# Optimization experiments

Measured on AMD Instinct MI355X. Metric: run time of the kernel, lower is better.

The kernel has to match this reference:

```python
import jax, jax.numpy as jnp
import numpy as np

K = 8            # NEAREST_K
IN = 68          # input_size = 64 + 4
EO = 32          # edge_output_size
FEAT = IN * 2 + EO * 4  # 264
EMB = 32         # linear_embedding
NCLS = 2
N = 768
EPS = 1e-5


def lrelu(x):
    return jnp.where(x >= 0, x, 0.01 * x)


def setup_inputs() -> dict:
    key = jax.random.key(0)
    ks = jax.random.split(key, 16)

    def w(k, fan_in, fan_out):
        return jax.random.normal(k, (fan_in, fan_out), jnp.float32) / np.float32(np.sqrt(fan_in))

    return {
        "feat0": jax.random.normal(ks[0], (N, IN), jnp.float32),
        "feat1": jax.random.normal(ks[1], (N, IN), jnp.float32),
        # edge_conv1: Linear(IN*K, EO) -> LeakyReLU -> Linear(EO, EO) -> LeakyReLU
        "ec1_w1": w(ks[2], IN * K, EO), "ec1_b1": jnp.zeros((EO,), jnp.float32),
        "ec1_w2": w(ks[3], EO, EO),     "ec1_b2": jnp.zeros((EO,), jnp.float32),
        # edge_conv2: Linear(EO*K, EO) -> LeakyReLU -> Linear(EO, EO) -> LeakyReLU
        "ec2_w1": w(ks[4], EO * K, EO), "ec2_b1": jnp.zeros((EO,), jnp.float32),
        "ec2_w2": w(ks[5], EO, EO),     "ec2_b2": jnp.zeros((EO,), jnp.float32),
        # linear head: BN(FEAT) -> Linear(FEAT,EMB) -> LReLU -> Linear(EMB,EMB) -> LReLU -> Linear(EMB,NCLS)
        "bn_g": jnp.ones((FEAT,), jnp.float32), "bn_b": jnp.zeros((FEAT,), jnp.float32),
        "lin1_w": w(ks[6], FEAT, EMB), "lin1_b": jnp.zeros((EMB,), jnp.float32),
        "lin2_w": w(ks[7], EMB, EMB),  "lin2_b": jnp.zeros((EMB,), jnp.float32),
        "lin3_w": w(ks[8], EMB, NCLS), "lin3_b": jnp.zeros((NCLS,), jnp.float32),
    }


def _pairs_for_graph(feat, ec1_w1, ec1_b1, ec1_w2, ec1_b2,
                     ec2_w1, ec2_b1, ec2_w2, ec2_b2):
    n = feat.shape[0]
    # kNN on first 4 dims via pairwise L1 distance (includes self, dist 0)
    coords = feat[:, :4]
    dist = jnp.abs(coords[:, None, :] - coords[None, :, :]).sum(-1)  # [n, n]
    _, idx = jax.lax.top_k(-dist, K)  # [n, K] smallest distances

    # EdgeConv 1: gather neighbor features, flatten feature-major (matches torch transpose+view)
    e1 = feat[idx]                                  # [n, K, IN]
    e1 = jnp.swapaxes(e1, 1, 2).reshape(n, IN * K)  # [n, IN*K]
    e1 = lrelu(lrelu(e1 @ ec1_w1 + ec1_b1) @ ec1_w2 + ec1_b2)  # [n, EO]

    # EdgeConv 2 on edge1 outputs
    e2 = e1[idx]                                    # [n, K, EO]
    e2 = jnp.swapaxes(e2, 1, 2).reshape(n, EO * K)  # [n, EO*K]
    e2 = lrelu(lrelu(e2 @ ec2_w1 + ec2_b1) @ ec2_w2 + ec2_b2)  # [n, EO]

    x = jnp.concatenate([feat, e1, e2], axis=-1)    # [n, IN + 2*EO] = [n, 132]
    # upper-triangle (i<j) all-pairs concat, row-major order == torch masked_select of triu mask
    iu, ju = jnp.triu_indices(n, k=1)
    return jnp.concatenate([x[iu], x[ju]], axis=-1)  # [n(n-1)/2, FEAT]


def reference(feat0, feat1, ec1_w1, ec1_b1, ec1_w2, ec1_b2,
              ec2_w1, ec2_b1, ec2_w2, ec2_b2,
              bn_g, bn_b, lin1_w, lin1_b, lin2_w, lin2_b, lin3_w, lin3_b):
    ec = (ec1_w1, ec1_b1, ec1_w2, ec1_b2, ec2_w1, ec2_b1, ec2_w2, ec2_b2)
    x = jnp.concatenate([_pairs_for_graph(feat0, *ec),
                         _pairs_for_graph(feat1, *ec)], axis=0)  # [P, FEAT]
    # BatchNorm1d in training mode: batch statistics (biased variance)
    mu = x.mean(axis=0)
    var = x.var(axis=0)
    x = (x - mu) * jax.lax.rsqrt(var + EPS) * bn_g + bn_b
    x = lrelu(x @ lin1_w + lin1_b)
    x = lrelu(x @ lin2_w + lin2_b)
    return x @ lin3_w + lin3_b  # [P, NCLS]
```

## Files before the change

### kernel.cpp

```cpp
#include <hip/hip_runtime.h>

#define NN 768
#define IN_F 68
#define KNN 8
#define EO 32
#define FEAT 264
#define HALF_FEAT 132
#define EMB 32
#define NPAIR 294528

typedef __attribute__((ext_vector_type(8))) short bf16x8;
typedef __attribute__((ext_vector_type(4))) float f32x4;

static __device__ __forceinline__ int pack_chop2(float x0, float x1) {
  return __builtin_amdgcn_perm(__float_as_uint(x1), __float_as_uint(x0), 0x07060302);
}
static __device__ __forceinline__ float chop(float x) {
  return __uint_as_float(__float_as_uint(x) & 0xffff0000u);
}

__global__ void __launch_bounds__(64) topk_ec1_kernel(
    const float* __restrict__ feat0, const float* __restrict__ feat1,
    const float* __restrict__ w1, const float* __restrict__ b1,
    const float* __restrict__ w2, const float* __restrict__ b2,
    int* __restrict__ idx_out, float* __restrict__ e1out)
{
  const int i = blockIdx.x, g = blockIdx.y;
  const float* __restrict__ feat = g ? feat1 : feat0;
  const int lane = threadIdx.x;

  __shared__ unsigned long long keys[64*8];
  __shared__ int nbr[8];
  __shared__ float gl[KNN*IN_F];
  __shared__ float hsh[EO];

  const float4 ci = *(const float4*)(feat + i*IN_F);

  float4 cand[12];
#pragma unroll
  for (int t = 0; t < 12; t++)
    cand[t] = *(const float4*)(feat + (lane + 64*t)*IN_F);

  float bd[8]; int bidx[8];
#pragma unroll
  for (int k = 0; k < 8; k++) { bd[k] = 1e30f; bidx[k] = 0; }
#pragma unroll
  for (int t = 0; t < 12; t++) {
    const int j = lane + 64*t;
    float d = fabsf(ci.x - cand[t].x);
    d += fabsf(ci.y - cand[t].y);
    d += fabsf(ci.z - cand[t].z);
    d += fabsf(ci.w - cand[t].w);
    if (d < bd[7]) {
#pragma unroll
      for (int k = 7; k >= 1; k--) {
        if (d < bd[k-1])    { bd[k] = bd[k-1]; bidx[k] = bidx[k-1]; }
        else if (d < bd[k]) { bd[k] = d;       bidx[k] = j; }
      }
      if (d < bd[0]) { bd[0] = d; bidx[0] = j; }
    }
  }
#pragma unroll
  for (int k = 0; k < 8; k++)
    keys[lane*8+k] = ((unsigned long long)__float_as_uint(bd[k]) << 32) | (unsigned)bidx[k];
  __syncthreads();
  int pos = 0;
#pragma unroll
  for (int r = 0; r < 8; r++) {
    unsigned long long mykey = keys[lane*8 + pos];
    unsigned long long mn = mykey;
#pragma unroll
    for (int s = 32; s >= 1; s >>= 1) {
      unsigned long long o = __shfl_xor(mn, s, 64);
      mn = (o < mn) ? o : mn;
    }
    if (mykey == mn) pos++;
    if (lane == 0) {
      int nb = (int)(mn & 0xffffffffull);
      nbr[r] = nb;
      idx_out[(g*NN+i)*8 + r] = nb;
    }
  }
  __syncthreads();

  for (int z = lane; z < KNN*17; z += 64) {
    int k = z / 17, q = z - k*17;
    *(float4*)&gl[k*IN_F + q*4] = *(const float4*)(feat + nbr[k]*IN_F + q*4);
  }
  __syncthreads();

  const int e = lane & 31, hf = lane >> 5;
  float ak[8];
#pragma unroll
  for (int k = 0; k < 8; k++) ak[k] = 0.f;
  const int cbeg = hf*34;
  for (int c = cbeg; c < cbeg+34; c++) {
#pragma unroll
    for (int k = 0; k < 8; k++)
      ak[k] += gl[k*IN_F+c] * w1[(c*8+k)*EO + e];
  }
  float acc = ((ak[0]+ak[1])+(ak[2]+ak[3])) + ((ak[4]+ak[5])+(ak[6]+ak[7]));
  acc += __shfl_xor(acc, 32, 64);
  if (hf == 0) {
    float h = acc + b1[e];
    hsh[e] = fmaxf(h, 0.01f*h);
  }
  __syncthreads();
  if (lane < 32) {
    float o0=0.f, o1=0.f, o2=0.f, o3=0.f;
#pragma unroll
    for (int m = 0; m < 32; m += 4) {
      o0 += hsh[m+0] * w2[(m+0)*EO + lane];
      o1 += hsh[m+1] * w2[(m+1)*EO + lane];
      o2 += hsh[m+2] * w2[(m+2)*EO + lane];
      o3 += hsh[m+3] * w2[(m+3)*EO + lane];
    }
    float o = b2[lane] + ((o0+o1)+(o2+o3));
    o = fmaxf(o, 0.01f*o);
    e1out[(g*NN+i)*EO + lane] = o;
  }
}

__global__ void __launch_bounds__(64) ec2_kernel(
    const int* __restrict__ idx, const float* __restrict__ e1,
    const float* __restrict__ w1, const float* __restrict__ b1,
    const float* __restrict__ w2, const float* __restrict__ b2,
    float* __restrict__ e2out)
{
  const int i = blockIdx.x, g = blockIdx.y;
  const int lane = threadIdx.x;
  __shared__ float gl[KNN*EO];
  __shared__ float hsh[EO];
  {
    const int k = lane >> 3, q = lane & 7;
    const int nb = idx[(g*NN+i)*8 + k];
    *(float4*)&gl[k*EO + q*4] = *(const float4*)(e1 + (g*NN+nb)*EO + q*4);
  }
  __syncthreads();
  const int e = lane & 31, hf = lane >> 5;
  float ak[8];
#pragma unroll
  for (int k = 0; k < 8; k++) ak[k] = 0.f;
  const int cbeg = hf*16;
  for (int c = cbeg; c < cbeg+16; c++) {
#pragma unroll
    for (int k = 0; k < 8; k++)
      ak[k] += gl[k*EO+c] * w1[(c*8+k)*EO + e];
  }
  float acc = ((ak[0]+ak[1])+(ak[2]+ak[3])) + ((ak[4]+ak[5])+(ak[6]+ak[7]));
  acc += __shfl_xor(acc, 32, 64);
  if (hf == 0) {
    float h = acc + b1[e];
    hsh[e] = fmaxf(h, 0.01f*h);
  }
  __syncthreads();
  if (lane < 32) {
    float o0=0.f, o1=0.f, o2=0.f, o3=0.f;
#pragma unroll
    for (int m = 0; m < 32; m += 4) {
      o0 += hsh[m+0] * w2[(m+0)*EO + lane];
      o1 += hsh[m+1] * w2[(m+1)*EO + lane];
      o2 += hsh[m+2] * w2[(m+2)*EO + lane];
      o3 += hsh[m+3] * w2[(m+3)*EO + lane];
    }
    float o = b2[lane] + ((o0+o1)+(o2+o3));
    o = fmaxf(o, 0.01f*o);
    e2out[(g*NN+i)*EO + lane] = o;
  }
}

__global__ void __launch_bounds__(256) stats_kernel(
    const float* __restrict__ feat0, const float* __restrict__ feat1,
    const float* __restrict__ e1, const float* __restrict__ e2,
    const float* __restrict__ bn_g,
    float* __restrict__ mu_out, float* __restrict__ sg_out)
{
  const int c = blockIdx.x;
  const int tid = threadIdx.x;
  double s1=0, s2=0, q1=0, q2=0;
  for (int t = tid; t < 2*NN; t += 256) {
    int g = t >= NN;
    int i = t - g*NN;
    float val;
    if (c < IN_F)      val = (g ? feat1 : feat0)[i*IN_F + c];
    else if (c < 100)  val = e1[(g*NN+i)*EO + (c-IN_F)];
    else               val = e2[(g*NN+i)*EO + (c-100)];
    double dv = val;
    double wf = (double)(NN-1-i), wsnd = (double)i;
    s1 += wf*dv;  s2 += wsnd*dv;
    double dq = dv*dv;
    q1 += wf*dq;  q2 += wsnd*dq;
  }
#pragma unroll
  for (int off = 32; off >= 1; off >>= 1) {
    s1 += __shfl_xor(s1, off, 64);
    s2 += __shfl_xor(s2, off, 64);
    q1 += __shfl_xor(q1, off, 64);
    q2 += __shfl_xor(q2, off, 64);
  }
  __shared__ double red[4][4];
  const int w = tid >> 6;
  if ((tid & 63) == 0) { red[w][0]=s1; red[w][1]=s2; red[w][2]=q1; red[w][3]=q2; }
  __syncthreads();
  if (tid == 0) {
    double t0 = red[0][0]+red[1][0]+red[2][0]+red[3][0];
    double t1 = red[0][1]+red[1][1]+red[2][1]+red[3][1];
    double t2 = red[0][2]+red[1][2]+red[2][2]+red[3][2];
    double t3 = red[0][3]+red[1][3]+red[2][3]+red[3][3];
    const double M2 = 2.0 * (double)NPAIR;
    double mu1 = t0/M2, mu2 = t1/M2;
    double v1 = t2/M2 - mu1*mu1;
    double v2 = t3/M2 - mu2*mu2;
    mu_out[c]           = (float)mu1;
    mu_out[HALF_FEAT+c] = (float)mu2;
    sg_out[c]           = (float)((double)bn_g[c] / sqrt(v1 + 1e-5));
    sg_out[HALF_FEAT+c] = (float)((double)bn_g[HALF_FEAT+c] / sqrt(v2 + 1e-5));
  }
}

__global__ void __launch_bounds__(64) uv_c0_kernel(
    const float* __restrict__ feat0, const float* __restrict__ feat1,
    const float* __restrict__ e1, const float* __restrict__ e2,
    const float* __restrict__ sg, const float* __restrict__ mu,
    const float* __restrict__ bn_b,
    const float* __restrict__ lin1_w, const float* __restrict__ lin1_b,
    float* __restrict__ u, float* __restrict__ v, float* __restrict__ c0g)
{
  const int i = blockIdx.x, g = blockIdx.y;
  const int t = threadIdx.x;
  if (i == NN) {
    if (g == 0 && t < EMB) {
      float a0=0.f, a1=0.f, a2=0.f, a3=0.f;
      for (int c = 0; c < FEAT; c += 4) {
        a0 += (bn_b[c+0] - mu[c+0]*sg[c+0]) * lin1_w[(c+0)*EMB + t];
        a1 += (bn_b[c+1] - mu[c+1]*sg[c+1]) * lin1_w[(c+1)*EMB + t];
        a2 += (bn_b[c+2] - mu[c+2]*sg[c+2]) * lin1_w[(c+2)*EMB + t];
        a3 += (bn_b[c+3] - mu[c+3]*sg[c+3]) * lin1_w[(c+3)*EMB + t];
      }
      c0g[t] = lin1_b[t] + ((a0+a1)+(a2+a3));
    }
    return;
  }
  __shared__ float x[HALF_FEAT];
  for (int c = t; c < IN_F; c += 64) x[c] = (g ? feat1 : feat0)[i*IN_F + c];
  if (t < 32) x[IN_F + t]     = e1[(g*NN+i)*EO + t];
  else        x[100 + (t-32)] = e2[(g*NN+i)*EO + (t-32)];
  __syncthreads();
  const int e = t & 31, hf = t >> 5;
  const int base = hf * HALF_FEAT;
  float a0=0.f, a1=0.f, a2=0.f, a3=0.f;
  for (int c = 0; c < HALF_FEAT; c += 4) {
    a0 += x[c+0] * sg[base+c+0] * lin1_w[(base+c+0)*EMB + e];
    a1 += x[c+1] * sg[base+c+1] * lin1_w[(base+c+1)*EMB + e];
    a2 += x[c+2] * sg[base+c+2] * lin1_w[(base+c+2)*EMB + e];
    a3 += x[c+3] * sg[base+c+3] * lin1_w[(base+c+3)*EMB + e];
  }
  float acc = ((a0+a1)+(a2+a3));
  float* dst = hf ? v : u;
  dst[(g*NN+i)*EMB + e] = acc;
}

__global__ void __launch_bounds__(256) pair_kernel(
    const float* __restrict__ u, const float* __restrict__ v,
    const float* __restrict__ c0g,
    const float* __restrict__ lin2_w, const float* __restrict__ lin2_b,
    const float* __restrict__ lin3_w, const float* __restrict__ lin3_b,
    float2* __restrict__ out)
{
  const int g = blockIdx.y;
  int rem = blockIdx.x;
  int a = 0;
  while (rem >= 48 - a) { rem -= 48 - a; a++; }
  const int b = a + rem;

  __shared__ float su[16*36], sv[16*36];
  __shared__ float wbuf[4][16*36];
  const int tid = threadIdx.x;
  {
    int r = tid >> 5, c = tid & 31;
    su[r*36+c] = u[(g*NN + a*16 + r)*EMB + c];
    sv[r*36+c] = v[(g*NN + b*16 + r)*EMB + c];
    r += 8;
    su[r*36+c] = u[(g*NN + a*16 + r)*EMB + c];
    sv[r*36+c] = v[(g*NN + b*16 + r)*EMB + c];
  }
  __syncthreads();

  const int lane = tid & 63, w = tid >> 6;
  const int q = lane & 15, kg = lane >> 4;

  union { int i[4]; bf16x8 v; } whi0, wlo0, whi1, wlo1;
#pragma unroll
  for (int d = 0; d < 4; d++) {
    float w0a = lin2_w[(kg*8+2*d)*32 + q],      w0b = lin2_w[(kg*8+2*d+1)*32 + q];
    float w1a = lin2_w[(kg*8+2*d)*32 + 16 + q], w1b = lin2_w[(kg*8+2*d+1)*32 + 16 + q];
    whi0.i[d] = pack_chop2(w0a, w0b);
    wlo0.i[d] = pack_chop2(w0a - chop(w0a), w0b - chop(w0b));
    whi1.i[d] = pack_chop2(w1a, w1b);
    wlo1.i[d] = pack_chop2(w1a - chop(w1a), w1b - chop(w1b));
  }
  float svc[8];
#pragma unroll
  for (int jj = 0; jj < 8; jj++)
    svc[jj] = sv[q*36 + kg*8 + jj] + c0g[kg*8+jj];
  float2 w3v[8]; float b2v[8];
#pragma unroll
  for (int jj = 0; jj < 8; jj++) {
    w3v[jj] = ((const float2*)lin3_w)[kg*8+jj];
    b2v[jj] = lin2_b[kg*8+jj];
  }
  const float b30 = lin3_b[0], b31 = lin3_b[1];

  float* wb = wbuf[w];
#pragma unroll
  for (int t = 0; t < 4; t++) {
    const int ty = w*4 + t;
    const float4 sa = *(const float4*)&su[ty*36 + kg*8];
    const float4 sb = *(const float4*)&su[ty*36 + kg*8 + 4];
    float se[8] = {sa.x, sa.y, sa.z, sa.w, sb.x, sb.y, sb.z, sb.w};
    union { int i[4]; bf16x8 v; } ahi, alo;
#pragma unroll
    for (int d = 0; d < 4; d++) {
      float s0 = se[2*d]   + svc[2*d];
      float s1 = se[2*d+1] + svc[2*d+1];
      s0 = fmaxf(s0, 0.01f*s0);
      s1 = fmaxf(s1, 0.01f*s1);
      ahi.i[d] = pack_chop2(s0, s1);
      alo.i[d] = pack_chop2(s0 - chop(s0), s1 - chop(s1));
    }
    f32x4 acc0 = {0.f,0.f,0.f,0.f}, acc1 = {0.f,0.f,0.f,0.f};
    acc0 = __builtin_amdgcn_mfma_f32_16x16x32_bf16(ahi.v, whi0.v, acc0, 0,0,0);
    acc1 = __builtin_amdgcn_mfma_f32_16x16x32_bf16(ahi.v, whi1.v, acc1, 0,0,0);
    acc0 = __builtin_amdgcn_mfma_f32_16x16x32_bf16(ahi.v, wlo0.v, acc0, 0,0,0);
    acc1 = __builtin_amdgcn_mfma_f32_16x16x32_bf16(ahi.v, wlo1.v, acc1, 0,0,0);
    acc0 = __builtin_amdgcn_mfma_f32_16x16x32_bf16(alo.v, whi0.v, acc0, 0,0,0);
    acc1 = __builtin_amdgcn_mfma_f32_16x16x32_bf16(alo.v, whi1.v, acc1, 0,0,0);
#pragma unroll
    for (int r = 0; r < 4; r++) {
      wb[(kg*4+r)*36 + q]      = acc0[r];
      wb[(kg*4+r)*36 + 16 + q] = acc1[r];
    }
    float o0 = 0.f, o1 = 0.f;
#pragma unroll
    for (int jj = 0; jj < 8; jj++) {
      float h = wb[q*36 + kg*8 + jj] + b2v[jj];
      h = fmaxf(h, 0.01f*h);
      o0 += h * w3v[jj].x;
      o1 += h * w3v[jj].y;
    }
    o0 += __shfl_xor(o0, 16, 64); o0 += __shfl_xor(o0, 32, 64);
    o1 += __shfl_xor(o1, 16, 64); o1 += __shfl_xor(o1, 32, 64);
    const int i = a*16 + ty, j = b*16 + q;
    if (lane < 16 && j > i) {
      long p = (long)i*NN - (long)i*(i+1)/2 + (j - i - 1);
      out[(long)g*NPAIR + p] = make_float2(o0 + b30, o1 + b31);
    }
  }
}

extern "C" void kernel_launch(void* const* d_in, const int* in_sizes, int n_in,
                              void* d_out, int out_size, void* d_ws, size_t ws_size,
                              hipStream_t stream)
{
  const float* feat0  = (const float*)d_in[0];
  const float* feat1  = (const float*)d_in[1];
  const float* ec1_w1 = (const float*)d_in[2];
  const float* ec1_b1 = (const float*)d_in[3];
  const float* ec1_w2 = (const float*)d_in[4];
  const float* ec1_b2 = (const float*)d_in[5];
  const float* ec2_w1 = (const float*)d_in[6];
  const float* ec2_b1 = (const float*)d_in[7];
  const float* ec2_w2 = (const float*)d_in[8];
  const float* ec2_b2 = (const float*)d_in[9];
  const float* bn_g   = (const float*)d_in[10];
  const float* bn_b   = (const float*)d_in[11];
  const float* lin1_w = (const float*)d_in[12];
  const float* lin1_b = (const float*)d_in[13];
  const float* lin2_w = (const float*)d_in[14];
  const float* lin2_b = (const float*)d_in[15];
  const float* lin3_w = (const float*)d_in[16];
  const float* lin3_b = (const float*)d_in[17];

  char* ws = (char*)d_ws;
  int*   idx = (int*)  (ws + 0);
  float* e1  = (float*)(ws + 49152);
  float* e2  = (float*)(ws + 245760);
  float* u   = (float*)(ws + 442368);
  float* v   = (float*)(ws + 638976);
  float* mu  = (float*)(ws + 835584);
  float* sg  = (float*)(ws + 836640);
  float* c0g = (float*)(ws + 837696);

  topk_ec1_kernel<<<dim3(768,2), 64, 0, stream>>>(feat0, feat1, ec1_w1, ec1_b1,
                                                  ec1_w2, ec1_b2, idx, e1);
  ec2_kernel<<<dim3(768,2), 64, 0, stream>>>(idx, e1, ec2_w1, ec2_b1,
                                             ec2_w2, ec2_b2, e2);
  stats_kernel<<<dim3(132), 256, 0, stream>>>(feat0, feat1, e1, e2, bn_g, mu, sg);
  uv_c0_kernel<<<dim3(769,2), 64, 0, stream>>>(feat0, feat1, e1, e2, sg, mu, bn_b,
                                               lin1_w, lin1_b, u, v, c0g);
  pair_kernel<<<dim3(1176,2), 256, 0, stream>>>(u, v, c0g, lin2_w, lin2_b,
                                                lin3_w, lin3_b, (float2*)d_out);
}
```

Before: 135.8 us.

## Move EdgeConv and lin1 projections onto split-bf16 MFMA, batch nodes per block

EdgeConv1, EdgeConv2 and the u/v lin1 projection now run as split-bf16 (hi/lo) MFMA matmuls instead of scalar FMA loops. Each block handles 4 nodes (16 for uv) with 256 threads, and waves split the K dimension and reduce through shared memory. The pair kernel's final lin3 reduction now uses register shuffles instead of a shared-memory round trip. The aim is to cut scalar FMA cost and the launch overhead of many tiny 64-thread blocks. The trade-off is more conversion work and fewer, larger blocks.

```diff
diff --git a/kernel.cpp b/kernel.cpp
--- a/kernel.cpp
+++ b/kernel.cpp
@@ -11,6 +11,7 @@
 
 typedef __attribute__((ext_vector_type(8))) short bf16x8;
 typedef __attribute__((ext_vector_type(4))) float f32x4;
+typedef __attribute__((ext_vector_type(4))) unsigned short u16x4;
 
 static __device__ __forceinline__ int pack_chop2(float x0, float x1) {
   return __builtin_amdgcn_perm(__float_as_uint(x1), __float_as_uint(x0), 0x07060302);
@@ -18,24 +19,32 @@
 static __device__ __forceinline__ float chop(float x) {
   return __uint_as_float(__float_as_uint(x) & 0xffff0000u);
 }
-
-__global__ void __launch_bounds__(64) topk_ec1_kernel(
+static __device__ __forceinline__ unsigned short bftrunc(float x) {
+  return (unsigned short)(__float_as_uint(x) >> 16);
+}
+static __device__ __forceinline__ float lrelu(float x) { return fmaxf(x, 0.01f*x); }
+
+#define MFMA(a,b,c) __builtin_amdgcn_mfma_f32_16x16x32_bf16((a),(b),(c),0,0,0)
+
+__global__ void __launch_bounds__(256) topk_ec1_kernel(
     const float* __restrict__ feat0, const float* __restrict__ feat1,
     const float* __restrict__ w1, const float* __restrict__ b1,
     const float* __restrict__ w2, const float* __restrict__ b2,
     int* __restrict__ idx_out, float* __restrict__ e1out)
 {
-  const int i = blockIdx.x, g = blockIdx.y;
+  const int bx = blockIdx.x, g = blockIdx.y;
   const float* __restrict__ feat = g ? feat1 : feat0;
-  const int lane = threadIdx.x;
-
-  __shared__ unsigned long long keys[64*8];
-  __shared__ int nbr[8];
-  __shared__ float gl[KNN*IN_F];
-  __shared__ float hsh[EO];
+  const int tid = threadIdx.x;
+  const int lane = tid & 63, w = tid >> 6;
+  const int i = bx*4 + w;
+
+  __shared__ unsigned long long keys[4][512];
+  __shared__ int nbr[4][8];
+  __shared__ unsigned short Ahi[4][544], Alo[4][544];
+  __shared__ float pbuf[4][4][32];
+  __shared__ unsigned short h1hi[4][32], h1lo[4][32];
 
   const float4 ci = *(const float4*)(feat + i*IN_F);
-
   float4 cand[12];
 #pragma unroll
   for (int t = 0; t < 12; t++)
@@ -62,12 +71,12 @@
   }
 #pragma unroll
   for (int k = 0; k < 8; k++)
-    keys[lane*8+k] = ((unsigned long long)__float_as_uint(bd[k]) << 32) | (unsigned)bidx[k];
+    keys[w][lane*8+k] = ((unsigned long long)__float_as_uint(bd[k]) << 32) | (unsigned)bidx[k];
   __syncthreads();
   int pos = 0;
 #pragma unroll
   for (int r = 0; r < 8; r++) {
-    unsigned long long mykey = keys[lane*8 + pos];
+    unsigned long long mykey = keys[w][lane*8 + pos];
     unsigned long long mn = mykey;
 #pragma unroll
     for (int s = 32; s >= 1; s >>= 1) {
@@ -77,95 +86,181 @@
     if (mykey == mn) pos++;
     if (lane == 0) {
       int nb = (int)(mn & 0xffffffffull);
-      nbr[r] = nb;
+      nbr[w][r] = nb;
       idx_out[(g*NN+i)*8 + r] = nb;
     }
   }
   __syncthreads();
 
-  for (int z = lane; z < KNN*17; z += 64) {
-    int k = z / 17, q = z - k*17;
-    *(float4*)&gl[k*IN_F + q*4] = *(const float4*)(feat + nbr[k]*IN_F + q*4);
-  }
-  __syncthreads();
-
-  const int e = lane & 31, hf = lane >> 5;
-  float ak[8];
-#pragma unroll
-  for (int k = 0; k < 8; k++) ak[k] = 0.f;
-  const int cbeg = hf*34;
-  for (int c = cbeg; c < cbeg+34; c++) {
-#pragma unroll
-    for (int k = 0; k < 8; k++)
-      ak[k] += gl[k*IN_F+c] * w1[(c*8+k)*EO + e];
-  }
-  float acc = ((ak[0]+ak[1])+(ak[2]+ak[3])) + ((ak[4]+ak[5])+(ak[6]+ak[7]));
-  acc += __shfl_xor(acc, 32, 64);
-  if (hf == 0) {
-    float h = acc + b1[e];
-    hsh[e] = fmaxf(h, 0.01f*h);
-  }
-  __syncthreads();
-  if (lane < 32) {
-    float o0=0.f, o1=0.f, o2=0.f, o3=0.f;
-#pragma unroll
-    for (int m = 0; m < 32; m += 4) {
-      o0 += hsh[m+0] * w2[(m+0)*EO + lane];
-      o1 += hsh[m+1] * w2[(m+1)*EO + lane];
-      o2 += hsh[m+2] * w2[(m+2)*EO + lane];
-      o3 += hsh[m+3] * w2[(m+3)*EO + lane];
-    }
-    float o = b2[lane] + ((o0+o1)+(o2+o3));
-    o = fmaxf(o, 0.01f*o);
-    e1out[(g*NN+i)*EO + lane] = o;
-  }
-}
-
-__global__ void __launch_bounds__(64) ec2_kernel(
+  for (int z = tid; z < 4*KNN*17; z += 256) {
+    int node = z / 136, rest = z - node*136;
+    int kn = rest / 17, c4 = (rest - kn*17) * 4;
+    float4 t = *(const float4*)(feat + nbr[node][kn]*IN_F + c4);
+    int kidx = kn*IN_F + c4;
+    u16x4 hi = { bftrunc(t.x), bftrunc(t.y), bftrunc(t.z), bftrunc(t.w) };
+    u16x4 lo = { bftrunc(t.x - chop(t.x)), bftrunc(t.y - chop(t.y)),
+                 bftrunc(t.z - chop(t.z)), bftrunc(t.w - chop(t.w)) };
+    *(u16x4*)&Ahi[node][kidx] = hi;
+    *(u16x4*)&Alo[node][kidx] = lo;
+  }
+  __syncthreads();
+
+  const int q = lane & 15, kg = lane >> 4;
+  f32x4 acc0 = {0.f,0.f,0.f,0.f}, acc1 = {0.f,0.f,0.f,0.f};
+  for (int cc = w; cc < 17; cc += 4) {
+    const int kb = cc*32 + kg*8;
+    bf16x8 ah = *(const bf16x8*)&Ahi[q & 3][kb];
+    bf16x8 al = *(const bf16x8*)&Alo[q & 3][kb];
+    union { int i[4]; bf16x8 v; } bh0, bl0, bh1, bl1;
+#pragma unroll
+    for (int d = 0; d < 4; d++) {
+      int k0 = kb + 2*d, k1 = k0 + 1;
+      int r0 = (k0 % IN_F)*8 + (k0 / IN_F);
+      int r1 = (k1 % IN_F)*8 + (k1 / IN_F);
+      float x0 = w1[r0*EO + q],      x1 = w1[r1*EO + q];
+      float y0 = w1[r0*EO + 16 + q], y1 = w1[r1*EO + 16 + q];
+      bh0.i[d] = pack_chop2(x0, x1);
+      bl0.i[d] = pack_chop2(x0 - chop(x0), x1 - chop(x1));
+      bh1.i[d] = pack_chop2(y0, y1);
+      bl1.i[d] = pack_chop2(y0 - chop(y0), y1 - chop(y1));
+    }
+    acc0 = MFMA(ah, bh0.v, acc0); acc0 = MFMA(ah, bl0.v, acc0); acc0 = MFMA(al, bh0.v, acc0);
+    acc1 = MFMA(ah, bh1.v, acc1); acc1 = MFMA(ah, bl1.v, acc1); acc1 = MFMA(al, bh1.v, acc1);
+  }
+  if (lane < 16) {
+#pragma unroll
+    for (int r = 0; r < 4; r++) { pbuf[w][r][q] = acc0[r]; pbuf[w][r][16+q] = acc1[r]; }
+  }
+  __syncthreads();
+  if (tid < 128) {
+    int node = tid >> 5, n = tid & 31;
+    float s = pbuf[0][node][n] + pbuf[1][node][n] + pbuf[2][node][n] + pbuf[3][node][n] + b1[n];
+    s = lrelu(s);
+    h1hi[node][n] = bftrunc(s);
+    h1lo[node][n] = bftrunc(s - chop(s));
+  }
+  __syncthreads();
+
+  {
+    bf16x8 ah = *(const bf16x8*)&h1hi[q & 3][kg*8];
+    bf16x8 al = *(const bf16x8*)&h1lo[q & 3][kg*8];
+    union { int i[4]; bf16x8 v; } bh0, bl0, bh1, bl1;
+#pragma unroll
+    for (int d = 0; d < 4; d++) {
+      int k0 = kg*8 + 2*d, k1 = k0 + 1;
+      float x0 = w2[k0*EO + q],      x1 = w2[k1*EO + q];
+      float y0 = w2[k0*EO + 16 + q], y1 = w2[k1*EO + 16 + q];
+      bh0.i[d] = pack_chop2(x0, x1);
+      bl0.i[d] = pack_chop2(x0 - chop(x0), x1 - chop(x1));
+      bh1.i[d] = pack_chop2(y0, y1);
+      bl1.i[d] = pack_chop2(y0 - chop(y0), y1 - chop(y1));
+    }
+    f32x4 c0 = {0.f,0.f,0.f,0.f}, c1 = {0.f,0.f,0.f,0.f};
+    c0 = MFMA(ah, bh0.v, c0); c0 = MFMA(ah, bl0.v, c0); c0 = MFMA(al, bh0.v, c0);
+    c1 = MFMA(ah, bh1.v, c1); c1 = MFMA(ah, bl1.v, c1); c1 = MFMA(al, bh1.v, c1);
+    if (lane < 16) {
+      float oA = lrelu(c0[w] + b2[q]);
+      float oB = lrelu(c1[w] + b2[16+q]);
+      e1out[(g*NN+i)*EO + q]      = oA;
+      e1out[(g*NN+i)*EO + 16 + q] = oB;
+    }
+  }
+}
+
+__global__ void __launch_bounds__(256) ec2_kernel(
     const int* __restrict__ idx, const float* __restrict__ e1,
     const float* __restrict__ w1, const float* __restrict__ b1,
     const float* __restrict__ w2, const float* __restrict__ b2,
     float* __restrict__ e2out)
 {
-  const int i = blockIdx.x, g = blockIdx.y;
-  const int lane = threadIdx.x;
-  __shared__ float gl[KNN*EO];
-  __shared__ float hsh[EO];
+  const int bx = blockIdx.x, g = blockIdx.y;
+  const int tid = threadIdx.x;
+  const int lane = tid & 63, w = tid >> 6;
+  const int i = bx*4 + w;
+
+  __shared__ int nbrL[4][8];
+  __shared__ unsigned short Ahi[4][256], Alo[4][256];
+  __shared__ float pbuf[4][4][32];
+  __shared__ unsigned short h1hi[4][32], h1lo[4][32];
+
+  if (tid < 32) {
+    int node = tid >> 3, kn = tid & 7;
+    nbrL[node][kn] = idx[(g*NN + bx*4 + node)*8 + kn];
+  }
+  __syncthreads();
+
   {
-    const int k = lane >> 3, q = lane & 7;
-    const int nb = idx[(g*NN+i)*8 + k];
-    *(float4*)&gl[k*EO + q*4] = *(const float4*)(e1 + (g*NN+nb)*EO + q*4);
-  }
-  __syncthreads();
-  const int e = lane & 31, hf = lane >> 5;
-  float ak[8];
-#pragma unroll
-  for (int k = 0; k < 8; k++) ak[k] = 0.f;
-  const int cbeg = hf*16;
-  for (int c = cbeg; c < cbeg+16; c++) {
-#pragma unroll
-    for (int k = 0; k < 8; k++)
-      ak[k] += gl[k*EO+c] * w1[(c*8+k)*EO + e];
-  }
-  float acc = ((ak[0]+ak[1])+(ak[2]+ak[3])) + ((ak[4]+ak[5])+(ak[6]+ak[7]));
-  acc += __shfl_xor(acc, 32, 64);
-  if (hf == 0) {
-    float h = acc + b1[e];
-    hsh[e] = fmaxf(h, 0.01f*h);
-  }
-  __syncthreads();
-  if (lane < 32) {
-    float o0=0.f, o1=0.f, o2=0.f, o3=0.f;
-#pragma unroll
-    for (int m = 0; m < 32; m += 4) {
-      o0 += hsh[m+0] * w2[(m+0)*EO + lane];
-      o1 += hsh[m+1] * w2[(m+1)*EO + lane];
-      o2 += hsh[m+2] * w2[(m+2)*EO + lane];
-      o3 += hsh[m+3] * w2[(m+3)*EO + lane];
-    }
-    float o = b2[lane] + ((o0+o1)+(o2+o3));
-    o = fmaxf(o, 0.01f*o);
-    e2out[(g*NN+i)*EO + lane] = o;
+    int z = tid;
+    int node = z >> 6, rest = z & 63;
+    int kn = rest >> 3, c4 = (rest & 7) * 4;
+    float4 t = *(const float4*)(e1 + (g*NN + nbrL[node][kn])*EO + c4);
+    int kidx = kn*EO + c4;
+    u16x4 hi = { bftrunc(t.x), bftrunc(t.y), bftrunc(t.z), bftrunc(t.w) };
+    u16x4 lo = { bftrunc(t.x - chop(t.x)), bftrunc(t.y - chop(t.y)),
+                 bftrunc(t.z - chop(t.z)), bftrunc(t.w - chop(t.w)) };
+    *(u16x4*)&Ahi[node][kidx] = hi;
+    *(u16x4*)&Alo[node][kidx] = lo;
+  }
+  __syncthreads();
+
+  const int q = lane & 15, kg = lane >> 4;
+  f32x4 acc0 = {0.f,0.f,0.f,0.f}, acc1 = {0.f,0.f,0.f,0.f};
+  for (int cc = w; cc < 8; cc += 4) {
+    const int kb = cc*32 + kg*8;
+    bf16x8 ah = *(const bf16x8*)&Ahi[q & 3][kb];
+    bf16x8 al = *(const bf16x8*)&Alo[q & 3][kb];
+    union { int i[4]; bf16x8 v; } bh0, bl0, bh1, bl1;
+#pragma unroll
+    for (int d = 0; d < 4; d++) {
+      int k0 = kb + 2*d, k1 = k0 + 1;
+      int r0 = ((k0 & 31) << 3) + (k0 >> 5);
+      int r1 = ((k1 & 31) << 3) + (k1 >> 5);
+      float x0 = w1[r0*EO + q],      x1 = w1[r1*EO + q];
+      float y0 = w1[r0*EO + 16 + q], y1 = w1[r1*EO + 16 + q];
+      bh0.i[d] = pack_chop2(x0, x1);
+      bl0.i[d] = pack_chop2(x0 - chop(x0), x1 - chop(x1));
+      bh1.i[d] = pack_chop2(y0, y1);
+      bl1.i[d] = pack_chop2(y0 - chop(y0), y1 - chop(y1));
+    }
+    acc0 = MFMA(ah, bh0.v, acc0); acc0 = MFMA(ah, bl0.v, acc0); acc0 = MFMA(al, bh0.v, acc0);
+    acc1 = MFMA(ah, bh1.v, acc1); acc1 = MFMA(ah, bl1.v, acc1); acc1 = MFMA(al, bh1.v, acc1);
+  }
+  if (lane < 16) {
+#pragma unroll
+    for (int r = 0; r < 4; r++) { pbuf[w][r][q] = acc0[r]; pbuf[w][r][16+q] = acc1[r]; }
+  }
+  __syncthreads();
+  if (tid < 128) {
+    int node = tid >> 5, n = tid & 31;
+    float s = pbuf[0][node][n] + pbuf[1][node][n] + pbuf[2][node][n] + pbuf[3][node][n] + b1[n];
+    s = lrelu(s);
+    h1hi[node][n] = bftrunc(s);
+    h1lo[node][n] = bftrunc(s - chop(s));
+  }
+  __syncthreads();
+  {
+    bf16x8 ah = *(const bf16x8*)&h1hi[q & 3][kg*8];
+    bf16x8 al = *(const bf16x8*)&h1lo[q & 3][kg*8];
+    union { int i[4]; bf16x8 v; } bh0, bl0, bh1, bl1;
+#pragma unroll
+    for (int d = 0; d < 4; d++) {
+      int k0 = kg*8 + 2*d, k1 = k0 + 1;
+      float x0 = w2[k0*EO + q],      x1 = w2[k1*EO + q];
+      float y0 = w2[k0*EO + 16 + q], y1 = w2[k1*EO + 16 + q];
+      bh0.i[d] = pack_chop2(x0, x1);
+      bl0.i[d] = pack_chop2(x0 - chop(x0), x1 - chop(x1));
+      bh1.i[d] = pack_chop2(y0, y1);
+      bl1.i[d] = pack_chop2(y0 - chop(y0), y1 - chop(y1));
+    }
+    f32x4 c0 = {0.f,0.f,0.f,0.f}, c1 = {0.f,0.f,0.f,0.f};
+    c0 = MFMA(ah, bh0.v, c0); c0 = MFMA(ah, bl0.v, c0); c0 = MFMA(al, bh0.v, c0);
+    c1 = MFMA(ah, bh1.v, c1); c1 = MFMA(ah, bl1.v, c1); c1 = MFMA(al, bh1.v, c1);
+    if (lane < 16) {
+      float oA = lrelu(c0[w] + b2[q]);
+      float oB = lrelu(c1[w] + b2[16+q]);
+      e2out[(g*NN+i)*EO + q]      = oA;
+      e2out[(g*NN+i)*EO + 16 + q] = oB;
+    }
   }
 }
 
@@ -218,7 +313,7 @@
   }
 }
 
-__global__ void __launch_bounds__(64) uv_c0_kernel(
+__global__ void __launch_bounds__(256) uv_kernel(
     const float* __restrict__ feat0, const float* __restrict__ feat1,
     const float* __restrict__ e1, const float* __restrict__ e2,
     const float* __restrict__ sg, const float* __restrict__ mu,
@@ -226,38 +321,101 @@
     const float* __restrict__ lin1_w, const float* __restrict__ lin1_b,
     float* __restrict__ u, float* __restrict__ v, float* __restrict__ c0g)
 {
-  const int i = blockIdx.x, g = blockIdx.y;
-  const int t = threadIdx.x;
-  if (i == NN) {
-    if (g == 0 && t < EMB) {
+  const int bx = blockIdx.x, g = blockIdx.y;
+  const int tid = threadIdx.x;
+  if (bx == 48) {
+    if (g == 0 && tid < EMB) {
       float a0=0.f, a1=0.f, a2=0.f, a3=0.f;
       for (int c = 0; c < FEAT; c += 4) {
-        a0 += (bn_b[c+0] - mu[c+0]*sg[c+0]) * lin1_w[(c+0)*EMB + t];
-        a1 += (bn_b[c+1] - mu[c+1]*sg[c+1]) * lin1_w[(c+1)*EMB + t];
-        a2 += (bn_b[c+2] - mu[c+2]*sg[c+2]) * lin1_w[(c+2)*EMB + t];
-        a3 += (bn_b[c+3] - mu[c+3]*sg[c+3]) * lin1_w[(c+3)*EMB + t];
+        a0 += (bn_b[c+0] - mu[c+0]*sg[c+0]) * lin1_w[(c+0)*EMB + tid];
+        a1 += (bn_b[c+1] - mu[c+1]*sg[c+1]) * lin1_w[(c+1)*EMB + tid];
+        a2 += (bn_b[c+2] - mu[c+2]*sg[c+2]) * lin1_w[(c+2)*EMB + tid];
+        a3 += (bn_b[c+3] - mu[c+3]*sg[c+3]) * lin1_w[(c+3)*EMB + tid];
       }
-      c0g[t] = lin1_b[t] + ((a0+a1)+(a2+a3));
+      c0g[tid] = lin1_b[tid] + ((a0+a1)+(a2+a3));
     }
     return;
   }
-  __shared__ float x[HALF_FEAT];
-  for (int c = t; c < IN_F; c += 64) x[c] = (g ? feat1 : feat0)[i*IN_F + c];
-  if (t < 32) x[IN_F + t]     = e1[(g*NN+i)*EO + t];
-  else        x[100 + (t-32)] = e2[(g*NN+i)*EO + (t-32)];
-  __syncthreads();
-  const int e = t & 31, hf = t >> 5;
-  const int base = hf * HALF_FEAT;
-  float a0=0.f, a1=0.f, a2=0.f, a3=0.f;
-  for (int c = 0; c < HALF_FEAT; c += 4) {
-    a0 += x[c+0] * sg[base+c+0] * lin1_w[(base+c+0)*EMB + e];
-    a1 += x[c+1] * sg[base+c+1] * lin1_w[(base+c+1)*EMB + e];
-    a2 += x[c+2] * sg[base+c+2] * lin1_w[(base+c+2)*EMB + e];
-    a3 += x[c+3] * sg[base+c+3] * lin1_w[(base+c+3)*EMB + e];
-  }
-  float acc = ((a0+a1)+(a2+a3));
-  float* dst = hf ? v : u;
-  dst[(g*NN+i)*EMB + e] = acc;
+  const float* __restrict__ feat = g ? feat1 : feat0;
+
+  __shared__ unsigned short Auh[16][160], Aul[16][160], Avh[16][160], Avl[16][160];
+  __shared__ float pbuf[2][4][16][32];
+
+  for (int z = tid; z < 16*33; z += 256) {
+    int node = z / 33, part = z - node*33;
+    int i = bx*16 + node;
+    float4 t; int k;
+    if (part < 17)      { t = *(const float4*)(feat + i*IN_F + part*4); k = part*4; }
+    else if (part < 25) { t = *(const float4*)(e1 + (g*NN+i)*EO + (part-17)*4); k = IN_F + (part-17)*4; }
+    else                { t = *(const float4*)(e2 + (g*NN+i)*EO + (part-25)*4); k = 100 + (part-25)*4; }
+    float4 s4 = *(const float4*)(sg + k);
+    float4 z4 = *(const float4*)(sg + HALF_FEAT + k);
+    float ux=t.x*s4.x, uy=t.y*s4.y, uz=t.z*s4.z, uw=t.w*s4.w;
+    float vx=t.x*z4.x, vy=t.y*z4.y, vz=t.z*z4.z, vw=t.w*z4.w;
+    u16x4 uh = { bftrunc(ux), bftrunc(uy), bftrunc(uz), bftrunc(uw) };
+    u16x4 ul = { bftrunc(ux-chop(ux)), bftrunc(uy-chop(uy)), bftrunc(uz-chop(uz)), bftrunc(uw-chop(uw)) };
+    u16x4 vh = { bftrunc(vx), bftrunc(vy), bftrunc(vz), bftrunc(vw) };
+    u16x4 vl = { bftrunc(vx-chop(vx)), bftrunc(vy-chop(vy)), bftrunc(vz-chop(vz)), bftrunc(vw-chop(vw)) };
+    *(u16x4*)&Auh[node][k] = uh;  *(u16x4*)&Aul[node][k] = ul;
+    *(u16x4*)&Avh[node][k] = vh;  *(u16x4*)&Avl[node][k] = vl;
+  }
+  if (tid < 112) {
+    int node = tid / 7, k = HALF_FEAT + (tid - node*7)*4;
+    u16x4 zz = {0,0,0,0};
+    *(u16x4*)&Auh[node][k] = zz; *(u16x4*)&Aul[node][k] = zz;
+    *(u16x4*)&Avh[node][k] = zz; *(u16x4*)&Avl[node][k] = zz;
+  }
+  __syncthreads();
+
+  const int lane = tid & 63, w = tid >> 6;
+  const int q = lane & 15, kg = lane >> 4;
+  f32x4 aU0 = {0.f,0.f,0.f,0.f}, aU1 = {0.f,0.f,0.f,0.f};
+  f32x4 aV0 = {0.f,0.f,0.f,0.f}, aV1 = {0.f,0.f,0.f,0.f};
+  for (int uu = w; uu < 10; uu += 4) {
+    int gm = uu / 5, cc = uu - gm*5;
+    const unsigned short* Ah = gm ? &Avh[0][0] : &Auh[0][0];
+    const unsigned short* Al = gm ? &Avl[0][0] : &Aul[0][0];
+    const int kb = cc*32 + kg*8;
+    bf16x8 ah = *(const bf16x8*)&Ah[q*160 + kb];
+    bf16x8 al = *(const bf16x8*)&Al[q*160 + kb];
+    union { int i[4]; bf16x8 v; } bh0, bl0, bh1, bl1;
+#pragma unroll
+    for (int d = 0; d < 4; d++) {
+      int k0 = kb + 2*d, k1 = k0 + 1;
+      int r0 = gm ? min(HALF_FEAT + k0, FEAT-1) : k0;
+      int r1 = gm ? min(HALF_FEAT + k1, FEAT-1) : k1;
+      float x0 = lin1_w[r0*EMB + q],      x1 = lin1_w[r1*EMB + q];
+      float y0 = lin1_w[r0*EMB + 16 + q], y1 = lin1_w[r1*EMB + 16 + q];
+      bh0.i[d] = pack_chop2(x0, x1);
+      bl0.i[d] = pack_chop2(x0 - chop(x0), x1 - chop(x1));
+      bh1.i[d] = pack_chop2(y0, y1);
+      bl1.i[d] = pack_chop2(y0 - chop(y0), y1 - chop(y1));
+    }
+    if (gm == 0) {
+      aU0 = MFMA(ah, bh0.v, aU0); aU0 = MFMA(ah, bl0.v, aU0); aU0 = MFMA(al, bh0.v, aU0);
+      aU1 = MFMA(ah, bh1.v, aU1); aU1 = MFMA(ah, bl1.v, aU1); aU1 = MFMA(al, bh1.v, aU1);
+    } else {
+      aV0 = MFMA(ah, bh0.v, aV0); aV0 = MFMA(ah, bl0.v, aV0); aV0 = MFMA(al, bh0.v, aV0);
+      aV1 = MFMA(ah, bh1.v, aV1); aV1 = MFMA(ah, bl1.v, aV1); aV1 = MFMA(al, bh1.v, aV1);
+    }
+  }
+#pragma unroll
+  for (int r = 0; r < 4; r++) {
+    pbuf[0][w][kg*4+r][q]    = aU0[r];
+    pbuf[0][w][kg*4+r][16+q] = aU1[r];
+    pbuf[1][w][kg*4+r][q]    = aV0[r];
+    pbuf[1][w][kg*4+r][16+q] = aV1[r];
+  }
+  __syncthreads();
+#pragma unroll
+  for (int t = 0; t < 4; t++) {
+    int z = tid + 256*t;
+    int gm = z >> 9, rest = z & 511, node = rest >> 5, n = rest & 31;
+    float s = pbuf[gm][0][node][n] + pbuf[gm][1][node][n]
+            + pbuf[gm][2][node][n] + pbuf[gm][3][node][n];
+    float* dst = gm ? v : u;
+    dst[(g*NN + bx*16 + node)*EMB + n] = s;
+  }
 }
 
 __global__ void __launch_bounds__(256) pair_kernel(
@@ -274,7 +432,6 @@
   const int b = a + rem;
 
   __shared__ float su[16*36], sv[16*36];
-  __shared__ float wbuf[4][16*36];
   const int tid = threadIdx.x;
   {
     int r = tid >> 5, c = tid & 31;
@@ -303,15 +460,11 @@
 #pragma unroll
   for (int jj = 0; jj < 8; jj++)
     svc[jj] = sv[q*36 + kg*8 + jj] + c0g[kg*8+jj];
-  float2 w3v[8]; float b2v[8];
-#pragma unroll
-  for (int jj = 0; jj < 8; jj++) {
-    w3v[jj] = ((const float2*)lin3_w)[kg*8+jj];
-    b2v[jj] = lin2_b[kg*8+jj];
-  }
+  const float b2a = lin2_b[q], b2b = lin2_b[16+q];
+  const float2 w3a = ((const float2*)lin3_w)[q];
+  const float2 w3b = ((const float2*)lin3_w)[16+q];
   const float b30 = lin3_b[0], b31 = lin3_b[1];
 
-  float* wb = wbuf[w];
 #pragma unroll
   for (int t = 0; t < 4; t++) {
     const int ty = w*4 + t;
@@ -323,37 +476,38 @@
     for (int d = 0; d < 4; d++) {
       float s0 = se[2*d]   + svc[2*d];
       float s1 = se[2*d+1] + svc[2*d+1];
-      s0 = fmaxf(s0, 0.01f*s0);
-      s1 = fmaxf(s1, 0.01f*s1);
+      s0 = lrelu(s0); s1 = lrelu(s1);
       ahi.i[d] = pack_chop2(s0, s1);
       alo.i[d] = pack_chop2(s0 - chop(s0), s1 - chop(s1));
     }
     f32x4 acc0 = {0.f,0.f,0.f,0.f}, acc1 = {0.f,0.f,0.f,0.f};
-    acc0 = __builtin_amdgcn_mfma_f32_16x16x32_bf16(ahi.v, whi0.v, acc0, 0,0,0);
-    acc1 = __builtin_amdgcn_mfma_f32_16x16x32_bf16(ahi.v, whi1.v, acc1, 0,0,0);
-    acc0 = __builtin_amdgcn_mfma_f32_16x16x32_bf16(ahi.v, wlo0.v, acc0, 0,0,0);
-    acc1 = __builtin_amdgcn_mfma_f32_16x16x32_bf16(ahi.v, wlo1.v, acc1, 0,0,0);
-    acc0 = __builtin_amdgcn_mfma_f32_16x16x32_bf16(alo.v, whi0.v, acc0, 0,0,0);
-    acc1 = __builtin_amdgcn_mfma_f32_16x16x32_bf16(alo.v, whi1.v, acc1, 0,0,0);
+    acc0 = MFMA(ahi.v, whi0.v, acc0); acc1 = MFMA(ahi.v, whi1.v, acc1);
+    acc0 = MFMA(ahi.v, wlo0.v, acc0); acc1 = MFMA(ahi.v, wlo1.v, acc1);
+    acc0 = MFMA(alo.v, whi0.v, acc0); acc1 = MFMA(alo.v, whi1.v, acc1);
+    float p0[4], p1[4];
 #pragma unroll
     for (int r = 0; r < 4; r++) {
-      wb[(kg*4+r)*36 + q]      = acc0[r];
-      wb[(kg*4+r)*36 + 16 + q] = acc1[r];
-    }
-    float o0 = 0.f, o1 = 0.f;
-#pragma unroll
-    for (int jj = 0; jj < 8; jj++) {
-      float h = wb[q*36 + kg*8 + jj] + b2v[jj];
-      h = fmaxf(h, 0.01f*h);
-      o0 += h * w3v[jj].x;
-      o1 += h * w3v[jj].y;
-    }
-    o0 += __shfl_xor(o0, 16, 64); o0 += __shfl_xor(o0, 32, 64);
-    o1 += __shfl_xor(o1, 16, 64); o1 += __shfl_xor(o1, 32, 64);
-    const int i = a*16 + ty, j = b*16 + q;
-    if (lane < 16 && j > i) {
-      long p = (long)i*NN - (long)i*(i+1)/2 + (j - i - 1);
-      out[(long)g*NPAIR + p] = make_float2(o0 + b30, o1 + b31);
+      float hA = lrelu(acc0[r] + b2a);
+      float hB = lrelu(acc1[r] + b2b);
+      p0[r] = hA*w3a.x + hB*w3b.x;
+      p1[r] = hA*w3a.y + hB*w3b.y;
+    }
+#pragma unroll
+    for (int s = 1; s <= 8; s <<= 1) {
+#pragma unroll
+      for (int r = 0; r < 4; r++) {
+        p0[r] += __shfl_xor(p0[r], s, 64);
+        p1[r] += __shfl_xor(p1[r], s, 64);
+      }
+    }
+    const int i = a*16 + ty;
+    if (q < 4) {
+      const int m = kg*4 + q;
+      const int j = b*16 + m;
+      if (j > i) {
+        long p = (long)i*NN - (long)i*(i+1)/2 + (j - i - 1);
+        out[(long)g*NPAIR + p] = make_float2(p0[q] + b30, p1[q] + b31);
+      }
     }
   }
 }
@@ -391,13 +545,13 @@
   float* sg  = (float*)(ws + 836640);
   float* c0g = (float*)(ws + 837696);
 
-  topk_ec1_kernel<<<dim3(768,2), 64, 0, stream>>>(feat0, feat1, ec1_w1, ec1_b1,
-                                                  ec1_w2, ec1_b2, idx, e1);
-  ec2_kernel<<<dim3(768,2), 64, 0, stream>>>(idx, e1, ec2_w1, ec2_b1,
-                                             ec2_w2, ec2_b2, e2);
+  topk_ec1_kernel<<<dim3(192,2), 256, 0, stream>>>(feat0, feat1, ec1_w1, ec1_b1,
+                                                   ec1_w2, ec1_b2, idx, e1);
+  ec2_kernel<<<dim3(192,2), 256, 0, stream>>>(idx, e1, ec2_w1, ec2_b1,
+                                              ec2_w2, ec2_b2, e2);
   stats_kernel<<<dim3(132), 256, 0, stream>>>(feat0, feat1, e1, e2, bn_g, mu, sg);
-  uv_c0_kernel<<<dim3(769,2), 64, 0, stream>>>(feat0, feat1, e1, e2, sg, mu, bn_b,
-                                               lin1_w, lin1_b, u, v, c0g);
+  uv_kernel<<<dim3(49,2), 256, 0, stream>>>(feat0, feat1, e1, e2, sg, mu, bn_b,
+                                            lin1_w, lin1_b, u, v, c0g);
   pair_kernel<<<dim3(1176,2), 256, 0, stream>>>(u, v, c0g, lin2_w, lin2_b,
                                                 lin3_w, lin3_b, (float2*)d_out);
 }
```

Measured after the change: 140.7 us. 3.6% more time.
